# Performance work log

Hardware: AMD Instinct MI355X
Metric: run time of the kernel (lower is better)

Reference implementation:

```python
import jax, jax.numpy as jnp
import numpy as np

N_BASIS = 16


def _kan_layer(x, coeffs, centers):
    # x: [b, in], coeffs: [out, in, n], centers: [n]
    mu = jnp.mean(x, axis=0)
    sd = jnp.std(x, axis=0, ddof=1)  # torch.std is unbiased by default
    xn = jnp.clip((x - mu) / (sd + 1e-6), -3.0, 3.0)
    # Gaussian RBF expansion: [b, in, n]
    basis = jnp.exp(-((xn[..., None] - centers) ** 2) / 0.5)
    return jnp.einsum('bin,oin->bo', basis, coeffs)


def setup_inputs() -> dict:
    key = jax.random.key(0)
    ks = jax.random.split(key, 6)
    B, IN, H = 16384, 256, 512
    return {
        'x': jax.random.normal(ks[0], (B, IN), jnp.float32),
        'coeffs1': jax.random.normal(ks[1], (H, IN, N_BASIS), jnp.float32) * 0.1,
        'coeffs2': jax.random.normal(ks[2], (H, H, N_BASIS), jnp.float32) * 0.1,
        'coeffs3': jax.random.normal(ks[3], (1, H, N_BASIS), jnp.float32) * 0.1,
        'skip_w': jax.random.normal(ks[4], (1, IN), jnp.float32) * 0.05,
        'skip_b': jnp.zeros((1,), jnp.float32),
    }


def reference(x, coeffs1, coeffs2, coeffs3, skip_w, skip_b):
    centers = jnp.linspace(-2.0, 2.0, N_BASIS).astype(x.dtype)
    h = jnp.tanh(_kan_layer(x, coeffs1, centers))
    h = jnp.tanh(_kan_layer(h, coeffs2, centers))
    out = _kan_layer(h, coeffs3, centers)[:, 0]  # squeeze(-1)
    skip = (x @ skip_w.T + skip_b)[:, 0]
    return out + skip
```

## Files before the change

kernel.cpp:

```cpp
#include <hip/hip_runtime.h>
#include <cstdint>
#include <cstddef>

typedef __attribute__((ext_vector_type(8))) _Float16 half8;
typedef __attribute__((ext_vector_type(4))) _Float16 half4;
typedef __attribute__((ext_vector_type(2))) __fp16   fp16x2;
typedef __attribute__((ext_vector_type(4))) float    floatx4;

static constexpr int B_ROWS = 16384;
static constexpr int IN_DIM = 256;
static constexpr int H_DIM  = 512;
static constexpr int NB     = 16;

__device__ __forceinline__ float fast_tanh(float x) {
  float ax = fabsf(x);
  float e  = __expf(2.0f * ax);
  float t  = 1.0f - 2.0f / (e + 1.0f);
  return copysignf(t, x);
}

__device__ __forceinline__ void gld16(const void* g, void* l) {
  __builtin_amdgcn_global_load_lds(
      (const __attribute__((address_space(1))) unsigned int*)g,
      (__attribute__((address_space(3))) unsigned int*)l, 16, 0, 0);
}

__global__ __launch_bounds__(256) void prep_k(const float* __restrict__ c1, _Float16* __restrict__ d1, size_t n41,
                                              const float* __restrict__ c2, _Float16* __restrict__ d2, size_t n42,
                                              const float* __restrict__ X,
                                              float* __restrict__ ps, float* __restrict__ ps2) {
  const int bx = blockIdx.x;
  if (bx < 128) {
    int c     = (bx & 3) * 64 + (threadIdx.x & 63);
    int chunk = threadIdx.x >> 6;
    int seg   = bx >> 2;
    int r0    = seg * 512;
    double s = 0.0, s2 = 0.0;
    for (int r = r0 + chunk; r < r0 + 512; r += 4) {
      float v = X[(size_t)r * IN_DIM + c];
      s += v; s2 += (double)v * (double)v;
    }
    __shared__ float Ls[256], Ls2[256];
    Ls[threadIdx.x] = (float)s; Ls2[threadIdx.x] = (float)s2;
    __syncthreads();
    if (chunk == 0) {
      int cl = threadIdx.x;
      float a  = Ls[cl]  + Ls[cl + 64]  + Ls[cl + 128]  + Ls[cl + 192];
      float b  = Ls2[cl] + Ls2[cl + 64] + Ls2[cl + 128] + Ls2[cl + 192];
      ps [(size_t)seg * IN_DIM + c] = a;
      ps2[(size_t)seg * IN_DIM + c] = b;
    }
  } else {
    size_t tot = n41 + n42;
    int nb_blocks = gridDim.x - 128;
    for (size_t i = (size_t)(bx - 128) * 256 + threadIdx.x; i < tot;
         i += (size_t)nb_blocks * 256) {
      const float4* sp; half4* dp; size_t j;
      if (i < n41) { sp = (const float4*)c1; dp = (half4*)d1; j = i; }
      else         { sp = (const float4*)c2; dp = (half4*)d2; j = i - n41; }
      float4 v = sp[j];
      int nb = (int)((j << 2) & 15);
      half4 r;
      float e0 = -2.f + (float)(nb + 0) * (4.f / 15.f);
      float e1 = -2.f + (float)(nb + 1) * (4.f / 15.f);
      float e2 = -2.f + (float)(nb + 2) * (4.f / 15.f);
      float e3 = -2.f + (float)(nb + 3) * (4.f / 15.f);
      r[0] = (_Float16)(v.x * __expf(-2.f * e0 * e0));
      r[1] = (_Float16)(v.y * __expf(-2.f * e1 * e1));
      r[2] = (_Float16)(v.z * __expf(-2.f * e2 * e2));
      r[3] = (_Float16)(v.w * __expf(-2.f * e3 * e3));
      dp[j] = r;
    }
  }
}

__global__ void stats_final_k(const float* __restrict__ ps,
                              const float* __restrict__ ps2,
                              int segs, int cols, int rows,
                              float* __restrict__ nmi, float* __restrict__ isd) {
  int c = blockIdx.x * blockDim.x + threadIdx.x;
  if (c >= cols) return;
  double s = 0.0, s2 = 0.0;
  for (int g = 0; g < segs; g++) { s += ps[(size_t)g * cols + c]; s2 += ps2[(size_t)g * cols + c]; }
  double mean = s / rows;
  double var  = (s2 - s * s / rows) / (rows - 1);
  if (var < 0.0) var = 0.0;
  float sd = (float)sqrt(var);
  float iv = 1.0f / (sd + 1e-6f);
  isd[c] = iv;
  nmi[c] = -(float)mean * iv;
}

__global__ __launch_bounds__(256, 2) void kan_gemm_fused(const float* __restrict__ X,
                                                         const float* __restrict__ nmi,
                                                         const float* __restrict__ isd,
                                                         const _Float16* __restrict__ Bm,
                                                         float* __restrict__ Hout,
                                                         float* __restrict__ psum,
                                                         float* __restrict__ psum2,
                                                         int C) {
  const int K = C << 4;
  const int steps = K >> 6;
  __shared__ __align__(16) _Float16 As[2][128 * 64];
  __shared__ __align__(16) _Float16 Bs[3][128 * 64];
  const int tid  = threadIdx.x;
  const int w = tid >> 6, lane = tid & 63;
  const int wm = w & 1, wn = w >> 1;
  const int lrow = lane & 15, quad = lane >> 4;
  const int row0 = blockIdx.x * 128;
  const int col0 = blockIdx.y * 128;

  const int s_row = tid >> 3;
  const int s_sl  = tid & 7;
  const int s_seg = s_sl ^ ((s_row >> 1) & 7);
  const _Float16* gB = Bm + (size_t)(col0 + s_row) * K + s_seg * 8;

  const int erow = tid >> 1, eh = tid & 1;
  const float* xp  = X   + (size_t)(row0 + erow) * C + 2 * eh;
  const float* mup = nmi + 2 * eh;
  const float* isp = isd + 2 * eh;

  floatx4 acc[4][4] = {};

  auto expand_store = [&](float2 v, float2 a, float2 b, int bufi) {
#pragma unroll
    for (int h = 0; h < 2; h++) {
      float xr = h ? v.y : v.x;
      float ii = h ? a.y : a.x;
      float bb = h ? b.y : b.x;
      float xn = fminf(fmaxf(fmaf(xr, ii, bb), -3.f), 3.f);
      float Wv = __expf(fmaf(-2.f, xn, -8.f) * xn);
      float g  = __expf((16.f / 15.f) * xn);
      float g2 = g * g, g4 = g2 * g2, g8 = g4 * g4;
      fp16x2 gg = __builtin_amdgcn_cvt_pkrtz(g2, g2);
      union { fp16x2 q[4]; half8 v8; } u0, u1;
      u0.q[0] = __builtin_amdgcn_cvt_pkrtz(Wv, Wv * g);
      u0.q[1] = u0.q[0] * gg;
      u0.q[2] = u0.q[1] * gg;
      u0.q[3] = u0.q[2] * gg;
      float W8 = Wv * g8;
      u1.q[0] = __builtin_amdgcn_cvt_pkrtz(W8, W8 * g);
      u1.q[1] = u1.q[0] * gg;
      u1.q[2] = u1.q[1] * gg;
      u1.q[3] = u1.q[2] * gg;
      int ks0 = 4 * eh + 2 * h;
      *(half8*)&As[bufi][(size_t)(ks0 * 128 + erow) * 8]       = u0.v8;
      *(half8*)&As[bufi][(size_t)((ks0 + 1) * 128 + erow) * 8] = u1.v8;
    }
  };

  float2 x0 = *(const float2*)xp;
  float2 a0 = *(const float2*)isp;
  float2 b0 = *(const float2*)mup;
#pragma unroll
  for (int i = 0; i < 4; i++)
    gld16(gB + (size_t)32 * i * K, &Bs[0][(size_t)(tid + 256 * i) * 8]);
  __builtin_amdgcn_sched_barrier(0);
#pragma unroll
  for (int i = 0; i < 4; i++)
    gld16(gB + 64 + (size_t)32 * i * K, &Bs[1][(size_t)(tid + 256 * i) * 8]);
  __builtin_amdgcn_sched_barrier(0);
  float2 xv = *(const float2*)(xp + 4);
  float2 av = *(const float2*)(isp + 4);
  float2 bv = *(const float2*)(mup + 4);
  expand_store(x0, a0, b0, 0);
  asm volatile("s_waitcnt vmcnt(7)" ::: "memory");
  asm volatile("s_waitcnt lgkmcnt(0)" ::: "memory");
  __builtin_amdgcn_s_barrier();
  __builtin_amdgcn_sched_barrier(0);

  int bcur = 0;
  for (int k = 0; k < steps; k++) {
    const int abuf = k & 1;
    const bool more  = (k + 1 < steps);
    const bool more2 = (k + 2 < steps);
    const int b2 = (bcur == 0) ? 2 : bcur - 1;
    if (more2) {
#pragma unroll
      for (int i = 0; i < 4; i++)
        gld16(gB + (size_t)(k + 2) * 64 + (size_t)32 * i * K,
              &Bs[b2][(size_t)(tid + 256 * i) * 8]);
      __builtin_amdgcn_sched_barrier(0);
    }
    half8 af0[4], bf0[4];
#pragma unroll
    for (int t = 0; t < 4; t++) {
      int arow = wm * 64 + t * 16 + lrow;
      af0[t] = *(const half8*)&As[abuf][(size_t)(quad * 128 + arow) * 8];
      int brow = wn * 64 + t * 16 + lrow;
      int bchunk = brow * 8 + (quad ^ ((brow >> 1) & 7));
      bf0[t] = *(const half8*)&Bs[bcur][(size_t)bchunk * 8];
    }
    __builtin_amdgcn_s_setprio(1);
#pragma unroll
    for (int tm = 0; tm < 4; tm++)
#pragma unroll
      for (int tn = 0; tn < 4; tn++)
        acc[tm][tn] = __builtin_amdgcn_mfma_f32_16x16x32_f16(af0[tm], bf0[tn], acc[tm][tn], 0, 0, 0);
    __builtin_amdgcn_s_setprio(0);
    if (more) {
      expand_store(xv, av, bv, abuf ^ 1);
      if (more2) {
        xv = *(const float2*)(xp + 4 * (k + 2));
        av = *(const float2*)(isp + 4 * (k + 2));
        bv = *(const float2*)(mup + 4 * (k + 2));
      }
    }
    half8 af1[4], bf1[4];
#pragma unroll
    for (int t = 0; t < 4; t++) {
      int arow = wm * 64 + t * 16 + lrow;
      af1[t] = *(const half8*)&As[abuf][(size_t)((4 + quad) * 128 + arow) * 8];
      int brow = wn * 64 + t * 16 + lrow;
      int bchunk = brow * 8 + ((4 + quad) ^ ((brow >> 1) & 7));
      bf1[t] = *(const half8*)&Bs[bcur][(size_t)bchunk * 8];
    }
    __builtin_amdgcn_s_setprio(1);
#pragma unroll
    for (int tm = 0; tm < 4; tm++)
#pragma unroll
      for (int tn = 0; tn < 4; tn++)
        acc[tm][tn] = __builtin_amdgcn_mfma_f32_16x16x32_f16(af1[tm], bf1[tn], acc[tm][tn], 0, 0, 0);
    __builtin_amdgcn_s_setprio(0);
    asm volatile("s_waitcnt lgkmcnt(0)" ::: "memory");
    __builtin_amdgcn_s_barrier();
    __builtin_amdgcn_sched_barrier(0);
    bcur = (bcur == 2) ? 0 : bcur + 1;
  }

  float* Rs1 = reinterpret_cast<float*>(&As[0][0]);
  float* Rs2 = Rs1 + 256;
  float s1[4] = {0.f, 0.f, 0.f, 0.f}, s2v[4] = {0.f, 0.f, 0.f, 0.f};
#pragma unroll
  for (int tm = 0; tm < 4; tm++) {
#pragma unroll
    for (int tn = 0; tn < 4; tn++) {
      int gcol = col0 + wn * 64 + tn * 16 + lrow;
#pragma unroll
      for (int r = 0; r < 4; r++) {
        int grow = row0 + wm * 64 + tm * 16 + quad * 4 + r;
        float v = fast_tanh(acc[tm][tn][r]);
        Hout[(size_t)grow * H_DIM + gcol] = v;
        s1[tn] += v; s2v[tn] += v * v;
      }
    }
  }
#pragma unroll
  for (int tn = 0; tn < 4; tn++) {
    s1[tn]  += __shfl_xor(s1[tn], 16);  s1[tn]  += __shfl_xor(s1[tn], 32);
    s2v[tn] += __shfl_xor(s2v[tn], 16); s2v[tn] += __shfl_xor(s2v[tn], 32);
  }
  if (quad == 0) {
#pragma unroll
    for (int tn = 0; tn < 4; tn++) {
      Rs1[wm * 128 + wn * 64 + tn * 16 + lrow] = s1[tn];
      Rs2[wm * 128 + wn * 64 + tn * 16 + lrow] = s2v[tn];
    }
  }
  asm volatile("s_waitcnt lgkmcnt(0)" ::: "memory");
  __builtin_amdgcn_s_barrier();
  __builtin_amdgcn_sched_barrier(0);
  if (tid < 128) {
    psum [(size_t)blockIdx.x * H_DIM + col0 + tid] = Rs1[tid] + Rs1[128 + tid];
    psum2[(size_t)blockIdx.x * H_DIM + col0 + tid] = Rs2[tid] + Rs2[128 + tid];
  }
}

__global__ __launch_bounds__(256) void layer3_k(const float* __restrict__ H2,
                                                const float* __restrict__ nmi,
                                                const float* __restrict__ isd,
                                                const float* __restrict__ C3,
                                                const float* __restrict__ X,
                                                const float* __restrict__ SW,
                                                const float* __restrict__ SB,
                                                float* __restrict__ OUT) {
  int w = threadIdx.x >> 6, lane = threadIdx.x & 63;
  float Kn[NB];
#pragma unroll
  for (int n = 0; n < NB; n++) {
    float c = -2.f + (float)n * (4.f / 15.f);
    Kn[n] = __expf(-2.f * c * c);
  }
  float sb0 = SB[0];
  int row_base = blockIdx.x * 16 + w * 4;
  for (int r = 0; r < 4; r++) {
    int row = row_base + r;
    float s = 0.f;
#pragma unroll
    for (int j = 0; j < 8; j++) {
      int i = lane + 64 * j;
      float hv = H2[(size_t)row * H_DIM + i];
      float xn = fminf(fmaxf(fmaf(hv, isd[i], nmi[i]), -3.f), 3.f);
      float Wf = __expf(fmaf(-2.f, xn, -8.f) * xn);
      float gf = __expf((16.f / 15.f) * xn);
      const floatx4* cp = (const floatx4*)(C3 + (size_t)i * NB);
      floatx4 c0 = cp[0], c1 = cp[1], c2 = cp[2], c3 = cp[3];
      float p = Wf;
#pragma unroll
      for (int n = 0; n < 4; n++) { s += p * Kn[n]      * c0[n]; p *= gf; }
#pragma unroll
      for (int n = 0; n < 4; n++) { s += p * Kn[n + 4]  * c1[n]; p *= gf; }
#pragma unroll
      for (int n = 0; n < 4; n++) { s += p * Kn[n + 8]  * c2[n]; p *= gf; }
#pragma unroll
      for (int n = 0; n < 4; n++) { s += p * Kn[n + 12] * c3[n]; p *= gf; }
    }
#pragma unroll
    for (int j = 0; j < 4; j++) {
      int i = lane + 64 * j;
      s += X[(size_t)row * IN_DIM + i] * SW[i];
    }
#pragma unroll
    for (int off = 32; off > 0; off >>= 1) s += __shfl_down(s, off);
    if (lane == 0) OUT[row] = s + sb0;
  }
}

extern "C" void kernel_launch(void* const* d_in, const int* in_sizes, int n_in,
                              void* d_out, int out_size, void* d_ws, size_t ws_size,
                              hipStream_t stream) {
  const float* x  = (const float*)d_in[0];
  const float* c1 = (const float*)d_in[1];
  const float* c2 = (const float*)d_in[2];
  const float* c3 = (const float*)d_in[3];
  const float* sw = (const float*)d_in[4];
  const float* sb = (const float*)d_in[5];
  float* out = (float*)d_out;

  const int B = B_ROWS, IN = IN_DIM, H = H_DIM;

  char* ws = (char*)d_ws;
  size_t off = 0;
  auto alloc = [&](size_t bytes) -> void* {
    void* p = ws + off;
    off += (bytes + 255) & ~(size_t)255;
    return p;
  };
  _Float16* C1h = (_Float16*)alloc((size_t)H * IN * NB * 2);
  _Float16* C2h = (_Float16*)alloc((size_t)H * H  * NB * 2);
  float* H1 = (float*)alloc((size_t)B * H * 4);
  float* H2 = (float*)alloc((size_t)B * H * 4);
  float* ps  = (float*)alloc(128 * 512 * 4);
  float* ps2 = (float*)alloc(128 * 512 * 4);
  float* nmi = (float*)alloc(512 * 4);
  float* isd = (float*)alloc(512 * 4);

  prep_k<<<128 + 1024, 256, 0, stream>>>(c1, C1h, (size_t)H * IN * NB / 4,
                                         c2, C2h, (size_t)H * H * NB / 4,
                                         x, ps, ps2);
  stats_final_k<<<1, 256, 0, stream>>>(ps, ps2, 32, IN, B, nmi, isd);

  kan_gemm_fused<<<dim3(B / 128, 4), 256, 0, stream>>>(x, nmi, isd, C1h, H1, ps, ps2, IN);
  stats_final_k<<<2, 256, 0, stream>>>(ps, ps2, 128, H, B, nmi, isd);

  kan_gemm_fused<<<dim3(B / 128, 4), 256, 0, stream>>>(H1, nmi, isd, C2h, H2, ps, ps2, H);
  stats_final_k<<<2, 256, 0, stream>>>(ps, ps2, 128, H, B, nmi, isd);

  layer3_k<<<B / 16, 256, 0, stream>>>(H2, nmi, isd, c3, x, sw, sb, out);
}
```

Before: 454.6 us.

## Double GEMM block to 512 threads with narrower per-wave tiles

Launches the fused KAN GEMM with 512 threads (8 waves) per block instead of 256. Each wave now computes a 64x32 output tile instead of 64x64. Each thread expands one input feature per K step instead of two, and issues two B-tile loads instead of four. The aim is more waves in flight to hide latency in the expansion and load pipeline. In exchange, each A fragment is re-read from LDS by more waves, so LDS traffic per MFMA rises, and the 512,4 launch bound may squeeze the register budget.

Result: no change. 457.6 us (+0.7%).

```diff
diff --git a/kernel.cpp b/kernel.cpp
--- a/kernel.cpp
+++ b/kernel.cpp
@@ -91,7 +91,7 @@
   nmi[c] = -(float)mean * iv;
 }
 
-__global__ __launch_bounds__(256, 2) void kan_gemm_fused(const float* __restrict__ X,
+__global__ __launch_bounds__(512, 4) void kan_gemm_fused(const float* __restrict__ X,
                                                          const float* __restrict__ nmi,
                                                          const float* __restrict__ isd,
                                                          const _Float16* __restrict__ Bm,
@@ -115,56 +115,49 @@
   const int s_seg = s_sl ^ ((s_row >> 1) & 7);
   const _Float16* gB = Bm + (size_t)(col0 + s_row) * K + s_seg * 8;
 
-  const int erow = tid >> 1, eh = tid & 1;
-  const float* xp  = X   + (size_t)(row0 + erow) * C + 2 * eh;
-  const float* mup = nmi + 2 * eh;
-  const float* isp = isd + 2 * eh;
-
-  floatx4 acc[4][4] = {};
-
-  auto expand_store = [&](float2 v, float2 a, float2 b, int bufi) {
-#pragma unroll
-    for (int h = 0; h < 2; h++) {
-      float xr = h ? v.y : v.x;
-      float ii = h ? a.y : a.x;
-      float bb = h ? b.y : b.x;
-      float xn = fminf(fmaxf(fmaf(xr, ii, bb), -3.f), 3.f);
-      float Wv = __expf(fmaf(-2.f, xn, -8.f) * xn);
-      float g  = __expf((16.f / 15.f) * xn);
-      float g2 = g * g, g4 = g2 * g2, g8 = g4 * g4;
-      fp16x2 gg = __builtin_amdgcn_cvt_pkrtz(g2, g2);
-      union { fp16x2 q[4]; half8 v8; } u0, u1;
-      u0.q[0] = __builtin_amdgcn_cvt_pkrtz(Wv, Wv * g);
-      u0.q[1] = u0.q[0] * gg;
-      u0.q[2] = u0.q[1] * gg;
-      u0.q[3] = u0.q[2] * gg;
-      float W8 = Wv * g8;
-      u1.q[0] = __builtin_amdgcn_cvt_pkrtz(W8, W8 * g);
-      u1.q[1] = u1.q[0] * gg;
-      u1.q[2] = u1.q[1] * gg;
-      u1.q[3] = u1.q[2] * gg;
-      int ks0 = 4 * eh + 2 * h;
-      *(half8*)&As[bufi][(size_t)(ks0 * 128 + erow) * 8]       = u0.v8;
-      *(half8*)&As[bufi][(size_t)((ks0 + 1) * 128 + erow) * 8] = u1.v8;
-    }
+  const int erow = tid & 127;
+  const int eh   = tid >> 7;
+  const float* xp  = X   + (size_t)(row0 + erow) * C + eh;
+  const float* mup = nmi + eh;
+  const float* isp = isd + eh;
+
+  floatx4 acc[4][2] = {};
+
+  auto expand_store = [&](float xr, float ii, float bb, int bufi) {
+    float xn = fminf(fmaxf(fmaf(xr, ii, bb), -3.f), 3.f);
+    float Wv = __expf(fmaf(-2.f, xn, -8.f) * xn);
+    float g  = __expf((16.f / 15.f) * xn);
+    float g2 = g * g, g4 = g2 * g2, g8 = g4 * g4;
+    fp16x2 gg = __builtin_amdgcn_cvt_pkrtz(g2, g2);
+    union { fp16x2 q[4]; half8 v8; } u0, u1;
+    u0.q[0] = __builtin_amdgcn_cvt_pkrtz(Wv, Wv * g);
+    u0.q[1] = u0.q[0] * gg;
+    u0.q[2] = u0.q[1] * gg;
+    u0.q[3] = u0.q[2] * gg;
+    float W8 = Wv * g8;
+    u1.q[0] = __builtin_amdgcn_cvt_pkrtz(W8, W8 * g);
+    u1.q[1] = u1.q[0] * gg;
+    u1.q[2] = u1.q[1] * gg;
+    u1.q[3] = u1.q[2] * gg;
+    int ks0 = 2 * eh;
+    *(half8*)&As[bufi][(size_t)(ks0 * 128 + erow) * 8]       = u0.v8;
+    *(half8*)&As[bufi][(size_t)((ks0 + 1) * 128 + erow) * 8] = u1.v8;
   };
 
-  float2 x0 = *(const float2*)xp;
-  float2 a0 = *(const float2*)isp;
-  float2 b0 = *(const float2*)mup;
-#pragma unroll
-  for (int i = 0; i < 4; i++)
-    gld16(gB + (size_t)32 * i * K, &Bs[0][(size_t)(tid + 256 * i) * 8]);
+  float x0 = xp[0];
+  float a0 = isp[0];
+  float b0 = mup[0];
+  gld16(gB, &Bs[0][(size_t)tid * 8]);
+  gld16(gB + (size_t)64 * K, &Bs[0][(size_t)(tid + 512) * 8]);
   __builtin_amdgcn_sched_barrier(0);
-#pragma unroll
-  for (int i = 0; i < 4; i++)
-    gld16(gB + 64 + (size_t)32 * i * K, &Bs[1][(size_t)(tid + 256 * i) * 8]);
+  gld16(gB + 64, &Bs[1][(size_t)tid * 8]);
+  gld16(gB + 64 + (size_t)64 * K, &Bs[1][(size_t)(tid + 512) * 8]);
   __builtin_amdgcn_sched_barrier(0);
-  float2 xv = *(const float2*)(xp + 4);
-  float2 av = *(const float2*)(isp + 4);
-  float2 bv = *(const float2*)(mup + 4);
+  float xv = xp[4];
+  float av = isp[4];
+  float bv = mup[4];
   expand_store(x0, a0, b0, 0);
-  asm volatile("s_waitcnt vmcnt(7)" ::: "memory");
+  asm volatile("s_waitcnt vmcnt(0)" ::: "memory");
   asm volatile("s_waitcnt lgkmcnt(0)" ::: "memory");
   __builtin_amdgcn_s_barrier();
   __builtin_amdgcn_sched_barrier(0);
@@ -176,18 +169,19 @@
     const bool more2 = (k + 2 < steps);
     const int b2 = (bcur == 0) ? 2 : bcur - 1;
     if (more2) {
-#pragma unroll
-      for (int i = 0; i < 4; i++)
-        gld16(gB + (size_t)(k + 2) * 64 + (size_t)32 * i * K,
-              &Bs[b2][(size_t)(tid + 256 * i) * 8]);
+      gld16(gB + (size_t)(k + 2) * 64, &Bs[b2][(size_t)tid * 8]);
+      gld16(gB + (size_t)(k + 2) * 64 + (size_t)64 * K, &Bs[b2][(size_t)(tid + 512) * 8]);
       __builtin_amdgcn_sched_barrier(0);
     }
-    half8 af0[4], bf0[4];
+    half8 af0[4], bf0[2];
 #pragma unroll
     for (int t = 0; t < 4; t++) {
       int arow = wm * 64 + t * 16 + lrow;
       af0[t] = *(const half8*)&As[abuf][(size_t)(quad * 128 + arow) * 8];
-      int brow = wn * 64 + t * 16 + lrow;
+    }
+#pragma unroll
+    for (int t = 0; t < 2; t++) {
+      int brow = wn * 32 + t * 16 + lrow;
       int bchunk = brow * 8 + (quad ^ ((brow >> 1) & 7));
       bf0[t] = *(const half8*)&Bs[bcur][(size_t)bchunk * 8];
     }
@@ -195,23 +189,26 @@
 #pragma unroll
     for (int tm = 0; tm < 4; tm++)
 #pragma unroll
-      for (int tn = 0; tn < 4; tn++)
+      for (int tn = 0; tn < 2; tn++)
         acc[tm][tn] = __builtin_amdgcn_mfma_f32_16x16x32_f16(af0[tm], bf0[tn], acc[tm][tn], 0, 0, 0);
     __builtin_amdgcn_s_setprio(0);
     if (more) {
       expand_store(xv, av, bv, abuf ^ 1);
       if (more2) {
-        xv = *(const float2*)(xp + 4 * (k + 2));
-        av = *(const float2*)(isp + 4 * (k + 2));
-        bv = *(const float2*)(mup + 4 * (k + 2));
+        xv = xp[4 * (k + 2)];
+        av = isp[4 * (k + 2)];
+        bv = mup[4 * (k + 2)];
       }
     }
-    half8 af1[4], bf1[4];
+    half8 af1[4], bf1[2];
 #pragma unroll
     for (int t = 0; t < 4; t++) {
       int arow = wm * 64 + t * 16 + lrow;
       af1[t] = *(const half8*)&As[abuf][(size_t)((4 + quad) * 128 + arow) * 8];
-      int brow = wn * 64 + t * 16 + lrow;
+    }
+#pragma unroll
+    for (int t = 0; t < 2; t++) {
+      int brow = wn * 32 + t * 16 + lrow;
       int bchunk = brow * 8 + ((4 + quad) ^ ((brow >> 1) & 7));
       bf1[t] = *(const half8*)&Bs[bcur][(size_t)bchunk * 8];
     }
@@ -219,7 +216,7 @@
 #pragma unroll
     for (int tm = 0; tm < 4; tm++)
 #pragma unroll
-      for (int tn = 0; tn < 4; tn++)
+      for (int tn = 0; tn < 2; tn++)
         acc[tm][tn] = __builtin_amdgcn_mfma_f32_16x16x32_f16(af1[tm], bf1[tn], acc[tm][tn], 0, 0, 0);
     __builtin_amdgcn_s_setprio(0);
     asm volatile("s_waitcnt lgkmcnt(0)" ::: "memory");
@@ -230,12 +227,12 @@
 
   float* Rs1 = reinterpret_cast<float*>(&As[0][0]);
   float* Rs2 = Rs1 + 256;
-  float s1[4] = {0.f, 0.f, 0.f, 0.f}, s2v[4] = {0.f, 0.f, 0.f, 0.f};
+  float s1[2] = {0.f, 0.f}, s2v[2] = {0.f, 0.f};
 #pragma unroll
   for (int tm = 0; tm < 4; tm++) {
 #pragma unroll
-    for (int tn = 0; tn < 4; tn++) {
-      int gcol = col0 + wn * 64 + tn * 16 + lrow;
+    for (int tn = 0; tn < 2; tn++) {
+      int gcol = col0 + wn * 32 + tn * 16 + lrow;
 #pragma unroll
       for (int r = 0; r < 4; r++) {
         int grow = row0 + wm * 64 + tm * 16 + quad * 4 + r;
@@ -246,15 +243,15 @@
     }
   }
 #pragma unroll
-  for (int tn = 0; tn < 4; tn++) {
+  for (int tn = 0; tn < 2; tn++) {
     s1[tn]  += __shfl_xor(s1[tn], 16);  s1[tn]  += __shfl_xor(s1[tn], 32);
     s2v[tn] += __shfl_xor(s2v[tn], 16); s2v[tn] += __shfl_xor(s2v[tn], 32);
   }
   if (quad == 0) {
 #pragma unroll
-    for (int tn = 0; tn < 4; tn++) {
-      Rs1[wm * 128 + wn * 64 + tn * 16 + lrow] = s1[tn];
-      Rs2[wm * 128 + wn * 64 + tn * 16 + lrow] = s2v[tn];
+    for (int tn = 0; tn < 2; tn++) {
+      Rs1[wm * 128 + wn * 32 + tn * 16 + lrow] = s1[tn];
+      Rs2[wm * 128 + wn * 32 + tn * 16 + lrow] = s2v[tn];
     }
   }
   asm volatile("s_waitcnt lgkmcnt(0)" ::: "memory");
@@ -350,10 +347,10 @@
                                          x, ps, ps2);
   stats_final_k<<<1, 256, 0, stream>>>(ps, ps2, 32, IN, B, nmi, isd);
 
-  kan_gemm_fused<<<dim3(B / 128, 4), 256, 0, stream>>>(x, nmi, isd, C1h, H1, ps, ps2, IN);
+  kan_gemm_fused<<<dim3(B / 128, 4), 512, 0, stream>>>(x, nmi, isd, C1h, H1, ps, ps2, IN);
   stats_final_k<<<2, 256, 0, stream>>>(ps, ps2, 128, H, B, nmi, isd);
 
-  kan_gemm_fused<<<dim3(B / 128, 4), 256, 0, stream>>>(H1, nmi, isd, C2h, H2, ps, ps2, H);
+  kan_gemm_fused<<<dim3(B / 128, 4), 512, 0, stream>>>(H1, nmi, isd, C2h, H2, ps, ps2, H);
   stats_final_k<<<2, 256, 0, stream>>>(ps, ps2, 128, H, B, nmi, isd);
 
   layer3_k<<<B / 16, 256, 0, stream>>>(H2, nmi, isd, c3, x, sw, sb, out);
```
